# Kernel tuning notes

Hardware: AMD Instinct MI355X
Metric: run time of the kernel (lower is better)

The kernel has to match this reference:

```python
import jax, jax.numpy as jnp
import numpy as np

PAD_IDX = 1
BATCH = 16
TLEN = 128
SLEN = 400          # full source length
AGENDA_LEN = 100    # slen_ in src_map
CONTEXT_LEN = SLEN - AGENDA_LEN
INPUT_SIZE = 1024
VOCAB = 32000
CVOCAB = 120


def setup_inputs() -> dict:
    key = jax.random.key(0)
    k1, k2, k3, k4, k5, k6, k7 = jax.random.split(key, 7)
    N = BATCH * TLEN
    hidden = jax.random.normal(k1, (N, INPUT_SIZE), dtype=jnp.float32)
    attn = jax.random.uniform(k2, (N, SLEN), dtype=jnp.float32)
    attn = attn / jnp.sum(attn, axis=1, keepdims=True)  # attention-like rows
    src_map = jax.random.uniform(k3, (AGENDA_LEN, BATCH, CVOCAB), dtype=jnp.float32)
    W = jax.random.normal(k4, (VOCAB, INPUT_SIZE), dtype=jnp.float32) * 0.02
    b = jnp.zeros((VOCAB,), dtype=jnp.float32)
    W_copy = jax.random.normal(k5, (1, INPUT_SIZE), dtype=jnp.float32) * 0.02
    b_copy = jnp.zeros((1,), dtype=jnp.float32)
    return {"hidden": hidden, "attn": attn, "src_map": src_map,
            "W": W, "b": b, "W_copy": W_copy, "b_copy": b_copy}


def reference(hidden, attn, src_map, W, b, W_copy, b_copy):
    # hidden: (tlen*batch, d), attn: (tlen*batch, slen), src_map: (agenda, batch, cvocab)
    agenda_len, batch, cvocab = src_map.shape
    slen = attn.shape[1]
    context_len = slen - agenda_len

    logits = hidden @ W.T + b                       # (N, vocab)
    logits = logits.at[:, PAD_IDX].set(-jnp.inf)
    prob = jax.nn.softmax(logits, axis=1)
    p_copy = jax.nn.sigmoid(hidden @ W_copy.T + b_copy)  # (N, 1)

    out_prob = prob * (1.0 - p_copy)                # (N, vocab)
    mul_attn = attn[:, context_len:] * p_copy       # (N, agenda)

    # rows are ordered (tlen, batch); bmm against per-batch indicator map
    ma = mul_attn.reshape(-1, batch, agenda_len)    # (tlen, batch, agenda)
    copy_prob = jnp.einsum('tba,abv->tbv', ma, src_map)  # (tlen, batch, cvocab)
    copy_prob = copy_prob.reshape(-1, cvocab)       # (N, cvocab)

    return jnp.concatenate([out_prob, copy_prob], axis=1), p_copy
```

## Files before the change

kernel.cpp:

```cpp
#include <hip/hip_runtime.h>

#define M_DIM 2048
#define K_DIM 1024
#define N_DIM 32000
#define CVOCAB 120
#define AGENDA 100
#define SLEN 400
#define CTX 300
#define BATCH 16
#define OUT_STRIDE 32120
#define PAD_IDX 1

#define TM 256
#define TN 256
#define BK 64
#define BUFSZ (TM * BK)
#define NKT (K_DIM / BK)
#define MT (M_DIM / TM)
#define NT (N_DIM / TN)

typedef float f32x4_t  __attribute__((ext_vector_type(4)));
typedef __bf16 bf16x8_t __attribute__((ext_vector_type(8)));
typedef unsigned short u16x8_t __attribute__((ext_vector_type(8)));
typedef unsigned short u16x4_t __attribute__((ext_vector_type(4)));

__device__ __forceinline__ unsigned short f2bf(float f) {
    union { float f; unsigned int u; } c; c.f = f;
    unsigned int u = c.u;
    u += 0x7FFFu + ((u >> 16) & 1u);
    return (unsigned short)(u >> 16);
}

__device__ __forceinline__ unsigned short f2h(float f) {
    _Float16 h = (_Float16)f;
    unsigned short u; __builtin_memcpy(&u, &h, 2); return u;
}
__device__ __forceinline__ float h2f(unsigned short u) {
    _Float16 h; __builtin_memcpy(&h, &u, 2); return (float)h;
}

__device__ __forceinline__ void async_copy16(const void* gsrc, void* ldst) {
    __builtin_amdgcn_global_load_lds(
        (__attribute__((address_space(1))) unsigned int*)(gsrc),
        (__attribute__((address_space(3))) unsigned int*)(ldst),
        16, 0, 0);
}

__global__ __launch_bounds__(256) void cast_bf16_kernel(
    const float4* __restrict__ W, const float4* __restrict__ H,
    unsigned short* __restrict__ Wb, unsigned short* __restrict__ Hb) {
    const size_t NW4 = (size_t)N_DIM * K_DIM / 4;
    const size_t NH4 = (size_t)M_DIM * K_DIM / 4;
    const size_t total = NW4 + NH4;
    const size_t stride = (size_t)gridDim.x * 256;
    for (size_t idx = (size_t)blockIdx.x * 256 + threadIdx.x; idx < total; idx += stride) {
        float4 v; unsigned short* dst;
        if (idx < NW4) { v = W[idx];        dst = Wb + idx * 4; }
        else           { v = H[idx - NW4];  dst = Hb + (idx - NW4) * 4; }
        u16x4_t o;
        o[0] = f2bf(v.x); o[1] = f2bf(v.y); o[2] = f2bf(v.z); o[3] = f2bf(v.w);
        *(u16x4_t*)dst = o;
    }
}

__global__ __launch_bounds__(256) void pcopy_copy_kernel(
    const float* __restrict__ hidden, const float* __restrict__ Wc,
    const float* __restrict__ bc, const float* __restrict__ attn,
    const float* __restrict__ src_map,
    float* __restrict__ out, float* __restrict__ out_tail,
    float* __restrict__ pcopy, float* __restrict__ rowsum) {
    const int row  = blockIdx.x * 4 + (threadIdx.x >> 6);
    const int lane = threadIdx.x & 63;
    const float4* h = (const float4*)(hidden + (size_t)row * K_DIM);
    const float4* w = (const float4*)Wc;
    float s = 0.f;
    #pragma unroll
    for (int i = 0; i < 4; ++i) {
        float4 a = h[lane + 64 * i];
        float4 b = w[lane + 64 * i];
        s += a.x * b.x + a.y * b.y + a.z * b.z + a.w * b.w;
    }
    #pragma unroll
    for (int m = 1; m < 64; m <<= 1) s += __shfl_xor(s, m);
    const float p = 1.0f / (1.0f + __expf(-(s + bc[0])));
    if (lane == 0) {
        pcopy[row]   = p;
        out_tail[row] = p;
        rowsum[row]  = 0.0f;
    }
    const int bidx = row & (BATCH - 1);
    const float* arow = attn + (size_t)row * SLEN + CTX;
    float s0 = 0.f, s1 = 0.f;
    #pragma unroll 4
    for (int a = 0; a < AGENDA; ++a) {
        float m = arow[a];
        const float* sm = src_map + (size_t)(a * BATCH + bidx) * CVOCAB;
        s0 += m * sm[lane];
        if (lane < CVOCAB - 64) s1 += m * sm[lane + 64];
    }
    float* orow = out + (size_t)row * OUT_STRIDE + N_DIM;
    orow[lane] = s0 * p;
    if (lane < CVOCAB - 64) orow[lane + 64] = s1 * p;
}

__global__ __launch_bounds__(1024, 4) void gemm_exp_kernel(
    const unsigned short* __restrict__ A,
    const unsigned short* __restrict__ B,
    const float* __restrict__ bias,
    unsigned short* __restrict__ E,
    const size_t eStride,
    float* __restrict__ rowsum)
{
    __shared__ unsigned short sA[2][BUFSZ];
    __shared__ unsigned short sB[2][BUFSZ];
    __shared__ float sRow[TM];

    const int tid   = threadIdx.x;
    const int lane  = tid & 63;
    const int q     = lane >> 4;
    const int lr    = lane & 15;
    const int wv    = tid >> 6;
    const int waveM = wv >> 2;
    const int waveN = wv & 3;

    const int bid = blockIdx.x;
    const int t   = (bid & 7) * NT + (bid >> 3);
    const int rowBase = (t & 7) * TM;
    const int colBase = (t >> 3) * TN;

    f32x4_t acc[4][4] = {};
    if (tid < TM) sRow[tid] = 0.0f;

    const int p0 = tid,        m0 = p0 >> 3, j0 = (p0 & 7) ^ (m0 & 7);
    const int p1 = 1024 + tid, m1 = p1 >> 3, j1 = (p1 & 7) ^ (m1 & 7);
    const unsigned short* aSrc0 = A + (size_t)(rowBase + m0) * K_DIM + j0 * 8;
    const unsigned short* aSrc1 = A + (size_t)(rowBase + m1) * K_DIM + j1 * 8;
    const unsigned short* bSrc0 = B + (size_t)(colBase + m0) * K_DIM + j0 * 8;
    const unsigned short* bSrc1 = B + (size_t)(colBase + m1) * K_DIM + j1 * 8;
    const int dOff0 = (tid & ~63) * 8;
    const int dOff1 = (1024 + (tid & ~63)) * 8;

    async_copy16(aSrc0, &sA[0][dOff0]);
    async_copy16(aSrc1, &sA[0][dOff1]);
    async_copy16(bSrc0, &sB[0][dOff0]);
    async_copy16(bSrc1, &sB[0][dOff1]);
    __syncthreads();

    for (int kt = 0; kt < NKT; ++kt) {
        const int cur = kt & 1;
        if (kt + 1 < NKT) {
            const int nb = cur ^ 1;
            const int k0 = (kt + 1) * BK;
            async_copy16(aSrc0 + k0, &sA[nb][dOff0]);
            async_copy16(aSrc1 + k0, &sA[nb][dOff1]);
            async_copy16(bSrc0 + k0, &sB[nb][dOff0]);
            async_copy16(bSrc1 + k0, &sB[nb][dOff1]);
        }
        const unsigned short* pA = sA[cur];
        const unsigned short* pB = sB[cur];
        #pragma unroll
        for (int s = 0; s < 2; ++s) {
            u16x8_t af[4], bfr[4];
            #pragma unroll
            for (int r = 0; r < 4; ++r) {
                int m  = waveM * 64 + r * 16 + lr;
                int ch = (s * 4 + q) ^ (m & 7);
                af[r] = *(const u16x8_t*)(pA + m * BK + ch * 8);
            }
            #pragma unroll
            for (int c = 0; c < 4; ++c) {
                int n  = waveN * 64 + c * 16 + lr;
                int ch = (s * 4 + q) ^ (n & 7);
                bfr[c] = *(const u16x8_t*)(pB + n * BK + ch * 8);
            }
            #pragma unroll
            for (int r = 0; r < 4; ++r)
                #pragma unroll
                for (int c = 0; c < 4; ++c)
                    acc[r][c] = __builtin_amdgcn_mfma_f32_16x16x32_bf16(
                        __builtin_bit_cast(bf16x8_t, af[r]),
                        __builtin_bit_cast(bf16x8_t, bfr[c]),
                        acc[r][c], 0, 0, 0);
        }
        __syncthreads();
    }

    float bb[4];
    #pragma unroll
    for (int c = 0; c < 4; ++c) bb[c] = bias[colBase + waveN * 64 + c * 16 + lr];

    #pragma unroll
    for (int r = 0; r < 4; ++r) {
        float rsum[4] = {0.f, 0.f, 0.f, 0.f};
        #pragma unroll
        for (int c = 0; c < 4; ++c) {
            int gcol = colBase + waveN * 64 + c * 16 + lr;
            bool pad = (gcol == PAD_IDX);
            #pragma unroll
            for (int d = 0; d < 4; ++d) {
                int grow = rowBase + waveM * 64 + r * 16 + q * 4 + d;
                float e = pad ? 0.0f : __expf(acc[r][c][d] + bb[c]);
                E[(size_t)grow * eStride + gcol] = f2h(e);
                rsum[d] += e;
            }
        }
        #pragma unroll
        for (int d = 0; d < 4; ++d) {
            float v = rsum[d];
            v += __shfl_xor(v, 1);
            v += __shfl_xor(v, 2);
            v += __shfl_xor(v, 4);
            v += __shfl_xor(v, 8);
            if (lr == 0) {
                int lrow = waveM * 64 + r * 16 + q * 4 + d;
                atomicAdd(&sRow[lrow], v);
            }
        }
    }
    __syncthreads();
    if (tid < TM) atomicAdd(&rowsum[rowBase + tid], sRow[tid]);
}

__global__ __launch_bounds__(256) void normalize_kernel(
    const unsigned short* __restrict__ E, float* __restrict__ out,
    const float* __restrict__ rowsum, const float* __restrict__ pcopy) {
    const int n   = blockIdx.x;
    const int tid = threadIdx.x;
    const float scale = (1.0f - pcopy[n]) / rowsum[n];
    const u16x8_t* src = (const u16x8_t*)(E + (size_t)n * N_DIM);
    float4* dst = (float4*)(out + (size_t)n * OUT_STRIDE);
    for (int j = tid; j < N_DIM / 8; j += 256) {
        u16x8_t h = src[j];
        float4 a, b;
        a.x = h2f(h[0]) * scale; a.y = h2f(h[1]) * scale;
        a.z = h2f(h[2]) * scale; a.w = h2f(h[3]) * scale;
        b.x = h2f(h[4]) * scale; b.y = h2f(h[5]) * scale;
        b.z = h2f(h[6]) * scale; b.w = h2f(h[7]) * scale;
        dst[j * 2]     = a;
        dst[j * 2 + 1] = b;
    }
}

__global__ __launch_bounds__(512) void normalize_inplace_kernel(
    float* __restrict__ out, const float* __restrict__ rowsum,
    const float* __restrict__ pcopy) {
    const int n   = blockIdx.x;
    const int tid = threadIdx.x;
    __shared__ unsigned short sE[N_DIM];
    const float scale = (1.0f - pcopy[n]) / rowsum[n];
    const u16x8_t* src = (const u16x8_t*)(out + (size_t)n * OUT_STRIDE);
    for (int j = tid; j < N_DIM / 8; j += 512)
        *(u16x8_t*)(sE + j * 8) = src[j];
    __syncthreads();
    float4* row4 = (float4*)(out + (size_t)n * OUT_STRIDE);
    for (int j = tid; j < N_DIM / 4; j += 512) {
        u16x4_t h = *(const u16x4_t*)(sE + j * 4);
        float4 v;
        v.x = h2f(h[0]) * scale;
        v.y = h2f(h[1]) * scale;
        v.z = h2f(h[2]) * scale;
        v.w = h2f(h[3]) * scale;
        row4[j] = v;
    }
}

extern "C" void kernel_launch(void* const* d_in, const int* in_sizes, int n_in,
                              void* d_out, int out_size, void* d_ws, size_t ws_size,
                              hipStream_t stream) {
    const float* hidden  = (const float*)d_in[0];
    const float* attn    = (const float*)d_in[1];
    const float* src_map = (const float*)d_in[2];
    const float* W       = (const float*)d_in[3];
    const float* b       = (const float*)d_in[4];
    const float* W_copy  = (const float*)d_in[5];
    const float* b_copy  = (const float*)d_in[6];
    float* out = (float*)d_out;

    char* ws = (char*)d_ws;
    unsigned short* Wb = (unsigned short*)ws;
    unsigned short* Hb = (unsigned short*)(ws + 65536000);
    float* rowsum      = (float*)(ws + 65536000 + 4194304);
    float* pcopy       = (float*)(ws + 65536000 + 4194304 + 8192);
    unsigned short* E  = (unsigned short*)(ws + 65536000 + 4194304 + 16384);
    const size_t wsNeeded = 65536000ull + 4194304 + 16384 + (size_t)M_DIM * N_DIM * 2;
    const bool useWsE = (ws_size >= wsNeeded);

    float* out_tail = out + (size_t)M_DIM * OUT_STRIDE;

    cast_bf16_kernel<<<2048, 256, 0, stream>>>((const float4*)W, (const float4*)hidden, Wb, Hb);
    pcopy_copy_kernel<<<M_DIM / 4, 256, 0, stream>>>(hidden, W_copy, b_copy, attn, src_map,
                                                     out, out_tail, pcopy, rowsum);
    if (useWsE) {
        gemm_exp_kernel<<<MT * NT, 1024, 0, stream>>>(Hb, Wb, b, E, (size_t)N_DIM, rowsum);
        normalize_kernel<<<M_DIM, 256, 0, stream>>>(E, out, rowsum, pcopy);
    } else {
        gemm_exp_kernel<<<MT * NT, 1024, 0, stream>>>(Hb, Wb, b, (unsigned short*)out,
                                                      (size_t)OUT_STRIDE * 2, rowsum);
        normalize_inplace_kernel<<<M_DIM, 512, 0, stream>>>(out, rowsum, pcopy);
    }
}
```

Baseline: 640.4 us.

## Fuse W bf16 cast into GEMM loads and drop separate cast and E buffer

Removes the standalone cast kernel. W is now loaded as fp32 in the GEMM main loop and converted to bf16 with v_cvt_pk_bf16_f32 before being stored into swizzled LDS. The hidden cast moves into the pcopy kernel, and exp values are always written in place into the output and then normalized through shared memory. This avoids writing and re-reading a 64MB bf16 copy of W and an extra E buffer. In exchange, each GEMM tile re-reads fp32 W (8 M-tiles per N column), which doubles B-operand global traffic and adds register-based conversion on the critical path instead of async LDS copies.

```diff
diff --git a/kernel.cpp b/kernel.cpp
--- a/kernel.cpp
+++ b/kernel.cpp
@@ -23,6 +23,7 @@
 typedef __bf16 bf16x8_t __attribute__((ext_vector_type(8)));
 typedef unsigned short u16x8_t __attribute__((ext_vector_type(8)));
 typedef unsigned short u16x4_t __attribute__((ext_vector_type(4)));
+typedef unsigned int   u32x4_t __attribute__((ext_vector_type(4)));
 
 __device__ __forceinline__ unsigned short f2bf(float f) {
     union { float f; unsigned int u; } c; c.f = f;
@@ -31,6 +32,12 @@
     return (unsigned short)(u >> 16);
 }
 
+__device__ __forceinline__ unsigned int cvt_pk_bf16(float lo, float hi) {
+    unsigned int r;
+    asm("v_cvt_pk_bf16_f32 %0, %1, %2" : "=v"(r) : "v"(lo), "v"(hi));
+    return r;
+}
+
 __device__ __forceinline__ unsigned short f2h(float f) {
     _Float16 h = (_Float16)f;
     unsigned short u; __builtin_memcpy(&u, &h, 2); return u;
@@ -46,27 +53,10 @@
         16, 0, 0);
 }
 
-__global__ __launch_bounds__(256) void cast_bf16_kernel(
-    const float4* __restrict__ W, const float4* __restrict__ H,
-    unsigned short* __restrict__ Wb, unsigned short* __restrict__ Hb) {
-    const size_t NW4 = (size_t)N_DIM * K_DIM / 4;
-    const size_t NH4 = (size_t)M_DIM * K_DIM / 4;
-    const size_t total = NW4 + NH4;
-    const size_t stride = (size_t)gridDim.x * 256;
-    for (size_t idx = (size_t)blockIdx.x * 256 + threadIdx.x; idx < total; idx += stride) {
-        float4 v; unsigned short* dst;
-        if (idx < NW4) { v = W[idx];        dst = Wb + idx * 4; }
-        else           { v = H[idx - NW4];  dst = Hb + (idx - NW4) * 4; }
-        u16x4_t o;
-        o[0] = f2bf(v.x); o[1] = f2bf(v.y); o[2] = f2bf(v.z); o[3] = f2bf(v.w);
-        *(u16x4_t*)dst = o;
-    }
-}
-
-__global__ __launch_bounds__(256) void pcopy_copy_kernel(
+__global__ __launch_bounds__(256) void pcopy_cast_kernel(
     const float* __restrict__ hidden, const float* __restrict__ Wc,
     const float* __restrict__ bc, const float* __restrict__ attn,
-    const float* __restrict__ src_map,
+    const float* __restrict__ src_map, unsigned short* __restrict__ Hb,
     float* __restrict__ out, float* __restrict__ out_tail,
     float* __restrict__ pcopy, float* __restrict__ rowsum) {
     const int row  = blockIdx.x * 4 + (threadIdx.x >> 6);
@@ -79,14 +69,17 @@
         float4 a = h[lane + 64 * i];
         float4 b = w[lane + 64 * i];
         s += a.x * b.x + a.y * b.y + a.z * b.z + a.w * b.w;
+        u16x4_t o;
+        o[0] = f2bf(a.x); o[1] = f2bf(a.y); o[2] = f2bf(a.z); o[3] = f2bf(a.w);
+        *(u16x4_t*)(Hb + (size_t)row * K_DIM + (lane + 64 * i) * 4) = o;
     }
     #pragma unroll
     for (int m = 1; m < 64; m <<= 1) s += __shfl_xor(s, m);
     const float p = 1.0f / (1.0f + __expf(-(s + bc[0])));
     if (lane == 0) {
-        pcopy[row]   = p;
+        pcopy[row]    = p;
         out_tail[row] = p;
-        rowsum[row]  = 0.0f;
+        rowsum[row]   = 0.0f;
     }
     const int bidx = row & (BATCH - 1);
     const float* arow = attn + (size_t)row * SLEN + CTX;
@@ -105,10 +98,9 @@
 
 __global__ __launch_bounds__(1024, 4) void gemm_exp_kernel(
     const unsigned short* __restrict__ A,
-    const unsigned short* __restrict__ B,
+    const float* __restrict__ Bf,
     const float* __restrict__ bias,
-    unsigned short* __restrict__ E,
-    const size_t eStride,
+    float* __restrict__ out,
     float* __restrict__ rowsum)
 {
     __shared__ unsigned short sA[2][BUFSZ];
@@ -135,26 +127,44 @@
     const int p1 = 1024 + tid, m1 = p1 >> 3, j1 = (p1 & 7) ^ (m1 & 7);
     const unsigned short* aSrc0 = A + (size_t)(rowBase + m0) * K_DIM + j0 * 8;
     const unsigned short* aSrc1 = A + (size_t)(rowBase + m1) * K_DIM + j1 * 8;
-    const unsigned short* bSrc0 = B + (size_t)(colBase + m0) * K_DIM + j0 * 8;
-    const unsigned short* bSrc1 = B + (size_t)(colBase + m1) * K_DIM + j1 * 8;
     const int dOff0 = (tid & ~63) * 8;
     const int dOff1 = (1024 + (tid & ~63)) * 8;
 
-    async_copy16(aSrc0, &sA[0][dOff0]);
-    async_copy16(aSrc1, &sA[0][dOff1]);
-    async_copy16(bSrc0, &sB[0][dOff0]);
-    async_copy16(bSrc1, &sB[0][dOff1]);
+    const int n_b = tid >> 2, j_b = tid & 3;
+    const float4* bRow = (const float4*)(Bf + (size_t)(colBase + n_b) * K_DIM);
+    const int csLo = j_b ^ (n_b & 7);
+    const int csHi = csLo ^ 4;
+    const int bOffLo = n_b * BK + csLo * 8;
+    const int bOffHi = n_b * BK + csHi * 8;
+
+#define CVT_STORE(DST, A4, B4) do {                        \
+        u32x4_t pk_;                                       \
+        pk_[0] = cvt_pk_bf16((A4).x, (A4).y);              \
+        pk_[1] = cvt_pk_bf16((A4).z, (A4).w);              \
+        pk_[2] = cvt_pk_bf16((B4).x, (B4).y);              \
+        pk_[3] = cvt_pk_bf16((B4).z, (B4).w);              \
+        *(u32x4_t*)(DST) = pk_; } while (0)
+
+    {
+        float4 l0 = bRow[j_b * 2], l1 = bRow[j_b * 2 + 1];
+        float4 l2 = bRow[j_b * 2 + 8], l3 = bRow[j_b * 2 + 9];
+        async_copy16(aSrc0, &sA[0][dOff0]);
+        async_copy16(aSrc1, &sA[0][dOff1]);
+        CVT_STORE(&sB[0][bOffLo], l0, l1);
+        CVT_STORE(&sB[0][bOffHi], l2, l3);
+    }
     __syncthreads();
 
     for (int kt = 0; kt < NKT; ++kt) {
-        const int cur = kt & 1;
+        const int cur = kt & 1, nb = cur ^ 1;
+        float4 l0, l1, l2, l3;
         if (kt + 1 < NKT) {
-            const int nb = cur ^ 1;
+            const int f4 = (kt + 1) * (BK / 4) + j_b * 2;
+            l0 = bRow[f4];     l1 = bRow[f4 + 1];
+            l2 = bRow[f4 + 8]; l3 = bRow[f4 + 9];
             const int k0 = (kt + 1) * BK;
             async_copy16(aSrc0 + k0, &sA[nb][dOff0]);
             async_copy16(aSrc1 + k0, &sA[nb][dOff1]);
-            async_copy16(bSrc0 + k0, &sB[nb][dOff0]);
-            async_copy16(bSrc1 + k0, &sB[nb][dOff1]);
         }
         const unsigned short* pA = sA[cur];
         const unsigned short* pB = sB[cur];
@@ -182,8 +192,13 @@
                         __builtin_bit_cast(bf16x8_t, bfr[c]),
                         acc[r][c], 0, 0, 0);
         }
+        if (kt + 1 < NKT) {
+            CVT_STORE(&sB[nb][bOffLo], l0, l1);
+            CVT_STORE(&sB[nb][bOffHi], l2, l3);
+        }
         __syncthreads();
     }
+#undef CVT_STORE
 
     float bb[4];
     #pragma unroll
@@ -200,7 +215,7 @@
             for (int d = 0; d < 4; ++d) {
                 int grow = rowBase + waveM * 64 + r * 16 + q * 4 + d;
                 float e = pad ? 0.0f : __expf(acc[r][c][d] + bb[c]);
-                E[(size_t)grow * eStride + gcol] = f2h(e);
+                ((unsigned short*)(out + (size_t)grow * OUT_STRIDE))[gcol] = f2h(e);
                 rsum[d] += e;
             }
         }
@@ -221,27 +236,7 @@
     if (tid < TM) atomicAdd(&rowsum[rowBase + tid], sRow[tid]);
 }
 
-__global__ __launch_bounds__(256) void normalize_kernel(
-    const unsigned short* __restrict__ E, float* __restrict__ out,
-    const float* __restrict__ rowsum, const float* __restrict__ pcopy) {
-    const int n   = blockIdx.x;
-    const int tid = threadIdx.x;
-    const float scale = (1.0f - pcopy[n]) / rowsum[n];
-    const u16x8_t* src = (const u16x8_t*)(E + (size_t)n * N_DIM);
-    float4* dst = (float4*)(out + (size_t)n * OUT_STRIDE);
-    for (int j = tid; j < N_DIM / 8; j += 256) {
-        u16x8_t h = src[j];
-        float4 a, b;
-        a.x = h2f(h[0]) * scale; a.y = h2f(h[1]) * scale;
-        a.z = h2f(h[2]) * scale; a.w = h2f(h[3]) * scale;
-        b.x = h2f(h[4]) * scale; b.y = h2f(h[5]) * scale;
-        b.z = h2f(h[6]) * scale; b.w = h2f(h[7]) * scale;
-        dst[j * 2]     = a;
-        dst[j * 2 + 1] = b;
-    }
-}
-
-__global__ __launch_bounds__(512) void normalize_inplace_kernel(
+__global__ __launch_bounds__(512) void finalize_kernel(
     float* __restrict__ out, const float* __restrict__ rowsum,
     const float* __restrict__ pcopy) {
     const int n   = blockIdx.x;
@@ -277,25 +272,15 @@
     float* out = (float*)d_out;
 
     char* ws = (char*)d_ws;
-    unsigned short* Wb = (unsigned short*)ws;
-    unsigned short* Hb = (unsigned short*)(ws + 65536000);
-    float* rowsum      = (float*)(ws + 65536000 + 4194304);
-    float* pcopy       = (float*)(ws + 65536000 + 4194304 + 8192);
-    unsigned short* E  = (unsigned short*)(ws + 65536000 + 4194304 + 16384);
-    const size_t wsNeeded = 65536000ull + 4194304 + 16384 + (size_t)M_DIM * N_DIM * 2;
-    const bool useWsE = (ws_size >= wsNeeded);
+    unsigned short* Hb = (unsigned short*)ws;
+    float* rowsum      = (float*)(ws + 4194304);
+    float* pcopy       = (float*)(ws + 4194304 + 8192);
 
     float* out_tail = out + (size_t)M_DIM * OUT_STRIDE;
 
-    cast_bf16_kernel<<<2048, 256, 0, stream>>>((const float4*)W, (const float4*)hidden, Wb, Hb);
-    pcopy_copy_kernel<<<M_DIM / 4, 256, 0, stream>>>(hidden, W_copy, b_copy, attn, src_map,
-                                                     out, out_tail, pcopy, rowsum);
-    if (useWsE) {
-        gemm_exp_kernel<<<MT * NT, 1024, 0, stream>>>(Hb, Wb, b, E, (size_t)N_DIM, rowsum);
-        normalize_kernel<<<M_DIM, 256, 0, stream>>>(E, out, rowsum, pcopy);
-    } else {
-        gemm_exp_kernel<<<MT * NT, 1024, 0, stream>>>(Hb, Wb, b, (unsigned short*)out,
-                                                      (size_t)OUT_STRIDE * 2, rowsum);
-        normalize_inplace_kernel<<<M_DIM, 512, 0, stream>>>(out, rowsum, pcopy);
-    }
-}
+    pcopy_cast_kernel<<<M_DIM / 4, 256, 0, stream>>>(hidden, W_copy, b_copy, attn,
+                                                     src_map, Hb, out, out_tail,
+                                                     pcopy, rowsum);
+    gemm_exp_kernel<<<MT * NT, 1024, 0, stream>>>(Hb, W, b, out, rowsum);
+    finalize_kernel<<<M_DIM, 512, 0, stream>>>(out, rowsum, pcopy);
+}
```

Measured after the change: 590.7 us. 7.8% less time.
